# Kernel tuning notes

Measured on AMD Instinct MI355X. Metric: run time of the kernel, lower is better.

The kernel has to match this reference:

```python
import jax, jax.numpy as jnp
import numpy as np

TEMP = 0.1
EPS = 1e-9  # torch CosineSimilarity eps


def setup_inputs() -> dict:
    key = jax.random.key(0)
    k1, k2 = jax.random.split(key)
    h = jax.random.normal(k1, (16384, 2048), dtype=jnp.float32)
    W = jax.random.normal(k2, (512, 2048), dtype=jnp.float32) * (1.0 / np.sqrt(2048))
    return {"h": h, "W": W}


def reference(h, W):
    # process_reps: h already 2D -> identity. Split into anchor / context halves.
    B = h.shape[0] // 2
    wz = h[:B] @ W.T      # [B, low_rank_dim]
    wc = h[B:] @ W.T      # [B, low_rank_dim]

    # CosineSimilarity(dim=-1, eps=1e-9): dot / max(||z||*||c||, eps), pairwise BxB
    nz = jnp.linalg.norm(wz, axis=-1)  # [B]
    nc = jnp.linalg.norm(wc, axis=-1)  # [B]
    sim = (wz @ wc.T) / jnp.maximum(nz[:, None] * nc[None, :], EPS)  # [B, B]
    sim = sim / TEMP

    sim_mean = sim.mean()
    sim_pos = jnp.diagonal(sim).mean()
    logprob = -jax.nn.log_softmax(sim, axis=1)
    loss = jnp.diagonal(logprob).mean()
    # matches loss_dict entries: {'loss', 'loss_pos', 'loss_neg'}
    return jnp.stack([loss, sim_pos, sim_mean])
```

## Files before the change

kernel.cpp:

```cpp
#include <hip/hip_runtime.h>


typedef __attribute__((ext_vector_type(8))) short bf16x8;
typedef __attribute__((ext_vector_type(4))) float floatx4;
typedef unsigned char uchar;

__device__ __forceinline__ unsigned short f2bf(float f) {
    union { float f; unsigned u; } v; v.f = f;
    unsigned r = (v.u + 0x7FFFu + ((v.u >> 16) & 1u)) >> 16;
    return (unsigned short)r;
}

__device__ __forceinline__ void async_copy16(const void* g, void* l) {
    __builtin_amdgcn_global_load_lds(
        (const __attribute__((address_space(1))) void*)g,
        (__attribute__((address_space(3))) void*)l,
        16, 0, 0);
}

__global__ __launch_bounds__(256) void cast_fp8_kernel(
    const float* __restrict__ src, uchar* __restrict__ dst, int n, float scale)
{
    const int i = (blockIdx.x * 256 + threadIdx.x) * 8;
    if (i + 7 < n) {
        float4 a = *reinterpret_cast<const float4*>(src + i);
        float4 b = *reinterpret_cast<const float4*>(src + i + 4);
        const int p01 = __builtin_amdgcn_cvt_pk_fp8_f32(a.x * scale, a.y * scale, 0, 0);
        const int p23 = __builtin_amdgcn_cvt_pk_fp8_f32(a.z * scale, a.w * scale, 0, 0);
        const int p45 = __builtin_amdgcn_cvt_pk_fp8_f32(b.x * scale, b.y * scale, 0, 0);
        const int p67 = __builtin_amdgcn_cvt_pk_fp8_f32(b.z * scale, b.w * scale, 0, 0);
        int2 w;
        w.x = (p01 & 0xffff) | (p23 << 16);
        w.y = (p45 & 0xffff) | (p67 << 16);
        *reinterpret_cast<int2*>(dst + i) = w;
    }
}

__device__ __forceinline__ size_t fl_off(int row_g, int col_g) {
    const int g = row_g >> 4, r15 = row_g & 15;
    const int c = col_g >> 5, q = (col_g >> 3) & 3, b = col_g & 7;
    return ((size_t)g * 16 + c) * 512 + (size_t)(q * 16 + r15) * 8 + b;
}

__global__ __launch_bounds__(256) void g1_main(
    const uchar* __restrict__ h8, const uchar* __restrict__ W8,
    uchar* __restrict__ Z8F, float* __restrict__ norm2)
{
    __shared__ __align__(16) uchar As[128 * 64];
    __shared__ __align__(16) uchar Bs[128 * 64];

    const int o = blockIdx.y * 4 + blockIdx.x;
    const int xcd = o & 7, idx = o >> 3;
    const int bn = idx & 3;
    const int bm = xcd * 16 + (idx >> 2);
    const int t = threadIdx.x;
    const int wave = t >> 6, lane = t & 63;
    const int wm = wave & 1, wn = wave >> 1;
    const int quad = lane >> 4, l15 = lane & 15;

    floatx4 acc[4][4];
    #pragma unroll
    for (int i = 0; i < 4; i++)
        #pragma unroll
        for (int j = 0; j < 4; j++) acc[i][j] = {0.f, 0.f, 0.f, 0.f};

    const int srow0 = wave * 32 + (lane >> 2);
    const int srow1 = srow0 + 16;
    const int p = lane & 3;
    const int sw0 = (p ^ ((srow0 >> 1) & 3)) << 4;
    const int sw1 = (p ^ ((srow1 >> 1) & 3)) << 4;
    const uchar* gA0 = h8 + (size_t)(bm * 128 + srow0) * 2048 + sw0;
    const uchar* gA1 = h8 + (size_t)(bm * 128 + srow1) * 2048 + sw1;
    const uchar* gB0 = W8 + (size_t)(bn * 128 + srow0) * 2048 + sw0;
    const uchar* gB1 = W8 + (size_t)(bn * 128 + srow1) * 2048 + sw1;
    uchar* lA0 = &As[(wave * 32 +  0) * 64];
    uchar* lA1 = &As[(wave * 32 + 16) * 64];
    uchar* lB0 = &Bs[(wave * 32 +  0) * 64];
    uchar* lB1 = &Bs[(wave * 32 + 16) * 64];

    for (int k0 = 0; k0 < 2048; k0 += 64) {
        async_copy16(gA0 + k0, lA0);
        async_copy16(gA1 + k0, lA1);
        async_copy16(gB0 + k0, lB0);
        async_copy16(gB1 + k0, lB1);
        __syncthreads();
        #pragma unroll
        for (int ch = 0; ch < 2; ch++) {
            const int s = ch * 2 + (quad >> 1);
            const int sub = (quad & 1) * 8;
            long a[4], b[4];
            #pragma unroll
            for (int i = 0; i < 4; i++) {
                const int row = wm * 64 + i * 16 + l15;
                a[i] = *reinterpret_cast<const long*>(
                    &As[row * 64 + ((s ^ ((row >> 1) & 3)) << 4) + sub]);
            }
            #pragma unroll
            for (int j = 0; j < 4; j++) {
                const int row = wn * 64 + j * 16 + l15;
                b[j] = *reinterpret_cast<const long*>(
                    &Bs[row * 64 + ((s ^ ((row >> 1) & 3)) << 4) + sub]);
            }
            #pragma unroll
            for (int i = 0; i < 4; i++)
                #pragma unroll
                for (int j = 0; j < 4; j++)
                    acc[i][j] = __builtin_amdgcn_mfma_f32_16x16x32_fp8_fp8(
                        a[i], b[j], acc[i][j], 0, 0, 0);
        }
        __syncthreads();
    }

    #pragma unroll
    for (int i = 0; i < 4; i++) {
        #pragma unroll
        for (int r = 0; r < 4; r++) {
            const int row_g = bm * 128 + wm * 64 + i * 16 + quad * 4 + r;
            const int pk01 = __builtin_amdgcn_cvt_pk_fp8_f32(acc[i][0][r], acc[i][1][r], 0, 0);
            const int pk23 = __builtin_amdgcn_cvt_pk_fp8_f32(acc[i][2][r], acc[i][3][r], 0, 0);
            const uchar q8[4] = { (uchar)(pk01 & 0xff), (uchar)((pk01 >> 8) & 0xff),
                                  (uchar)(pk23 & 0xff), (uchar)((pk23 >> 8) & 0xff) };
            #pragma unroll
            for (int j = 0; j < 4; j++) {
                const int col_g = bn * 128 + wn * 64 + j * 16 + l15;
                Z8F[fl_off(row_g, col_g)] = q8[j];
            }
            const float q0 = __builtin_amdgcn_cvt_f32_fp8(pk01, 0);
            const float q1 = __builtin_amdgcn_cvt_f32_fp8(pk01, 1);
            const float q2 = __builtin_amdgcn_cvt_f32_fp8(pk23, 0);
            const float q3 = __builtin_amdgcn_cvt_f32_fp8(pk23, 1);
            float pw = q0 * q0 + q1 * q1 + q2 * q2 + q3 * q3;
            pw += __shfl_xor(pw, 1, 16);
            pw += __shfl_xor(pw, 2, 16);
            pw += __shfl_xor(pw, 4, 16);
            pw += __shfl_xor(pw, 8, 16);
            if (l15 == 0) atomicAdd(&norm2[row_g], pw);
        }
    }
}

__global__ __launch_bounds__(256) void g1_slow(
    const float* __restrict__ h, const float* __restrict__ W,
    uchar* __restrict__ Z8F, float* __restrict__ norm2)
{
    __shared__ __align__(16) unsigned short As[128][40];
    __shared__ __align__(16) unsigned short Bs[128][40];

    const int bn = blockIdx.x, bm = blockIdx.y;
    const int t = threadIdx.x;
    const int wave = t >> 6, lane = t & 63;
    const int wm = wave & 1, wn = wave >> 1;
    const int quad = lane >> 4, l15 = lane & 15;

    floatx4 acc[4][4];
    #pragma unroll
    for (int i = 0; i < 4; i++)
        #pragma unroll
        for (int j = 0; j < 4; j++) acc[i][j] = {0.f, 0.f, 0.f, 0.f};

    const int lrow = t >> 1, lhalf = t & 1;
    const float* ga = h + (size_t)(bm * 128 + lrow) * 2048 + lhalf * 16;
    const float* gb = W + (size_t)(bn * 128 + lrow) * 2048 + lhalf * 16;

    for (int k0 = 0; k0 < 2048; k0 += 32) {
        #pragma unroll
        for (int c = 0; c < 4; c++) {
            const float4 va = *reinterpret_cast<const float4*>(ga + k0 + c * 4);
            const float4 vb = *reinterpret_cast<const float4*>(gb + k0 + c * 4);
            ushort4 ua = make_ushort4(f2bf(va.x), f2bf(va.y), f2bf(va.z), f2bf(va.w));
            ushort4 ub = make_ushort4(f2bf(vb.x), f2bf(vb.y), f2bf(vb.z), f2bf(vb.w));
            *reinterpret_cast<ushort4*>(&As[lrow][lhalf * 16 + c * 4]) = ua;
            *reinterpret_cast<ushort4*>(&Bs[lrow][lhalf * 16 + c * 4]) = ub;
        }
        __syncthreads();
        bf16x8 af[4], bfr[4];
        #pragma unroll
        for (int i = 0; i < 4; i++)
            af[i] = *reinterpret_cast<const bf16x8*>(&As[wm * 64 + i * 16 + l15][quad * 8]);
        #pragma unroll
        for (int j = 0; j < 4; j++)
            bfr[j] = *reinterpret_cast<const bf16x8*>(&Bs[wn * 64 + j * 16 + l15][quad * 8]);
        #pragma unroll
        for (int i = 0; i < 4; i++)
            #pragma unroll
            for (int j = 0; j < 4; j++)
                acc[i][j] = __builtin_amdgcn_mfma_f32_16x16x32_bf16(af[i], bfr[j], acc[i][j], 0, 0, 0);
        __syncthreads();
    }

    #pragma unroll
    for (int i = 0; i < 4; i++) {
        #pragma unroll
        for (int r = 0; r < 4; r++) {
            const int row_g = bm * 128 + wm * 64 + i * 16 + quad * 4 + r;
            const int pk01 = __builtin_amdgcn_cvt_pk_fp8_f32(acc[i][0][r], acc[i][1][r], 0, 0);
            const int pk23 = __builtin_amdgcn_cvt_pk_fp8_f32(acc[i][2][r], acc[i][3][r], 0, 0);
            const uchar q8[4] = { (uchar)(pk01 & 0xff), (uchar)((pk01 >> 8) & 0xff),
                                  (uchar)(pk23 & 0xff), (uchar)((pk23 >> 8) & 0xff) };
            #pragma unroll
            for (int j = 0; j < 4; j++) {
                const int col_g = bn * 128 + wn * 64 + j * 16 + l15;
                Z8F[fl_off(row_g, col_g)] = q8[j];
            }
            const float q0 = __builtin_amdgcn_cvt_f32_fp8(pk01, 0);
            const float q1 = __builtin_amdgcn_cvt_f32_fp8(pk01, 1);
            const float q2 = __builtin_amdgcn_cvt_f32_fp8(pk23, 0);
            const float q3 = __builtin_amdgcn_cvt_f32_fp8(pk23, 1);
            float pw = q0 * q0 + q1 * q1 + q2 * q2 + q3 * q3;
            pw += __shfl_xor(pw, 1, 16);
            pw += __shfl_xor(pw, 2, 16);
            pw += __shfl_xor(pw, 4, 16);
            pw += __shfl_xor(pw, 8, 16);
            if (l15 == 0) atomicAdd(&norm2[row_g], pw);
        }
    }
}

__global__ __launch_bounds__(256, 4) void g2_main(
    const uchar* __restrict__ Z8F, const float* __restrict__ norm2,
    float* __restrict__ rowse, float* __restrict__ bsum, float* __restrict__ bdiag)
{
    __shared__ float lds_red[2][128][19];
    __shared__ float red[8];

    const int o = blockIdx.y * 64 + blockIdx.x;
    const int xcd = o & 7, idx = o >> 3;
    const int bg = idx >> 7, r = idx & 127;
    const int bm = xcd * 8 + (r >> 4);
    const int bn = bg * 16 + (r & 15);
    const int t = threadIdx.x;
    const int wave = t >> 6, lane = t & 63;
    const int wm = wave & 1, wn = wave >> 1;
    const int quad = lane >> 4, l15 = lane & 15;

    floatx4 acc[4][4];
    #pragma unroll
    for (int i = 0; i < 4; i++)
        #pragma unroll
        for (int j = 0; j < 4; j++) acc[i][j] = {0.f, 0.f, 0.f, 0.f};

    const uchar* baseA = Z8F + ((size_t)(bm * 8 + wm * 4) * 16) * 512 + lane * 8;
    const uchar* baseB = Z8F + ((size_t)(512 + bn * 8 + wn * 4) * 16) * 512 + lane * 8;

    long a[2][4], b[2][4];
    #pragma unroll
    for (int i = 0; i < 4; i++) {
        a[0][i] = *reinterpret_cast<const long*>(baseA + i * 8192);
        b[0][i] = *reinterpret_cast<const long*>(baseB + i * 8192);
    }
    #pragma unroll
    for (int c = 0; c < 16; c++) {
        const int cur = c & 1, nxt = cur ^ 1;
        if (c < 15) {
            #pragma unroll
            for (int i = 0; i < 4; i++) {
                a[nxt][i] = *reinterpret_cast<const long*>(baseA + i * 8192 + (c + 1) * 512);
                b[nxt][i] = *reinterpret_cast<const long*>(baseB + i * 8192 + (c + 1) * 512);
            }
        }
        __builtin_amdgcn_s_setprio(1);
        #pragma unroll
        for (int i = 0; i < 4; i++)
            #pragma unroll
            for (int j = 0; j < 4; j++)
                acc[i][j] = __builtin_amdgcn_mfma_f32_16x16x32_fp8_fp8(
                    a[cur][i], b[cur][j], acc[i][j], 0, 0, 0);
        __builtin_amdgcn_s_setprio(0);
    }

    float rc4[4];
    #pragma unroll
    for (int j = 0; j < 4; j++)
        rc4[j] = rsqrtf(fmaxf(norm2[8192 + bn * 128 + wn * 64 + j * 16 + l15], 1e-30f));

    const bool diagblk = (bm == bn) && (wm == wn);
    float s_tot2 = 0.f, s_diag2 = 0.f;
    #pragma unroll
    for (int i = 0; i < 4; i++) {
        #pragma unroll
        for (int rr = 0; rr < 4; rr++) {
            const int row_t = wm * 64 + i * 16 + quad * 4 + rr;
            const float rzl2 = rsqrtf(fmaxf(norm2[bm * 128 + row_t], 1e-30f)) * 14.4269504089f;
            float rx = 0.f;
            #pragma unroll
            for (int j = 0; j < 4; j++) {
                const float sim2 = acc[i][j][rr] * rzl2 * rc4[j];
                s_tot2 += sim2;
                rx += exp2f(sim2);
            }
            lds_red[wn][row_t][l15] = rx;
            if (diagblk) {
                const float sdv = acc[i][i][rr] * rzl2 * rc4[i];
                s_diag2 += (l15 == quad * 4 + rr) ? sdv : 0.f;
            }
        }
    }
    __syncthreads();

    {
        const int row_t = t >> 1, part = t & 1;
        float v = 0.f;
        #pragma unroll
        for (int c = 0; c < 16; c++) v += lds_red[part][row_t][c];
        v += __shfl_xor(v, 1, 64);
        if (part == 0) atomicAdd(&rowse[bm * 128 + row_t], v);
    }

    #pragma unroll
    for (int off = 32; off; off >>= 1) {
        s_tot2  += __shfl_xor(s_tot2, off, 64);
        s_diag2 += __shfl_xor(s_diag2, off, 64);
    }
    if (lane == 0) { red[wave] = s_tot2; red[4 + wave] = s_diag2; }
    __syncthreads();
    if (t == 0) {
        bsum[bm * 64 + bn]  = (red[0] + red[1] + red[2] + red[3]) * 0.69314718056f;
        bdiag[bm * 64 + bn] = (red[4] + red[5] + red[6] + red[7]) * 0.69314718056f;
    }
}

__global__ __launch_bounds__(256) void finalize_kernel(
    const float* __restrict__ rowse, const float* __restrict__ bsum,
    const float* __restrict__ bdiag, float* __restrict__ out)
{
    float a = 0.f, b = 0.f, c = 0.f;
    for (int i = threadIdx.x; i < 8192; i += 256) a += logf(rowse[i]);
    for (int i = threadIdx.x; i < 4096; i += 256) { b += bsum[i]; c += bdiag[i]; }
    #pragma unroll
    for (int off = 32; off; off >>= 1) {
        a += __shfl_xor(a, off, 64);
        b += __shfl_xor(b, off, 64);
        c += __shfl_xor(c, off, 64);
    }
    __shared__ float ra[4], rb[4], rc[4];
    const int wave = threadIdx.x >> 6, lane = threadIdx.x & 63;
    if (lane == 0) { ra[wave] = a; rb[wave] = b; rc[wave] = c; }
    __syncthreads();
    if (threadIdx.x == 0) {
        const float A = ra[0] + ra[1] + ra[2] + ra[3];
        const float B = rb[0] + rb[1] + rb[2] + rb[3];
        const float C = rc[0] + rc[1] + rc[2] + rc[3];
        const float diag_mean = C / 8192.f;
        out[0] = A / 8192.f - diag_mean;
        out[1] = diag_mean;
        out[2] = B / (8192.f * 8192.f);
    }
}

extern "C" void kernel_launch(void* const* d_in, const int* in_sizes, int n_in,
                              void* d_out, int out_size, void* d_ws, size_t ws_size,
                              hipStream_t stream) {
    const float* h = (const float*)d_in[0];
    const float* W = (const float*)d_in[1];
    float* out = (float*)d_out;

    char* ws = (char*)d_ws;
    float* norm2 = (float*)(ws);
    float* rowse = (float*)(ws + 65536);
    float* bsum  = (float*)(ws + 98304);
    float* bdiag = (float*)(ws + 114688);
    uchar* Z8F   = (uchar*)(ws + 131072);
    uchar* W8    = (uchar*)(ws + 8519680);
    uchar* h8    = (uchar*)(ws + 9568256);
    const size_t NEED_FAST = 43122688ull;

    hipMemsetAsync(ws, 0, 131072, stream);

    if (ws_size >= NEED_FAST) {
        const int nh = 16384 * 2048, nw = 512 * 2048;
        hipLaunchKernelGGL(cast_fp8_kernel, dim3(nh / 2048), dim3(256), 0, stream, h, h8, nh, 1.0f);
        hipLaunchKernelGGL(cast_fp8_kernel, dim3(nw / 2048), dim3(256), 0, stream, W, W8, nw, 32.0f);
        hipLaunchKernelGGL(g1_main, dim3(4, 128), dim3(256), 0, stream, h8, W8, Z8F, norm2);
    } else {
        hipLaunchKernelGGL(g1_slow, dim3(4, 128), dim3(256), 0, stream, h, W, Z8F, norm2);
    }
    hipLaunchKernelGGL(g2_main, dim3(64, 64), dim3(256), 0, stream, Z8F, norm2, rowse, bsum, bdiag);
    hipLaunchKernelGGL(finalize_kernel, dim3(1), dim3(256), 0, stream, rowse, bsum, bdiag, out);
}
```

Measured before the change: 316.5 us.

## Stage B tile in LDS via async copies and repartition waves along M

Each wave previously loaded its own A and B fragments straight from global memory in a 2x2 wave grid. Now the whole 128-row B tile is staged into LDS with async global-to-LDS copies in two halves over K, so all four waves share it. Each wave owns 32 rows of A across all 128 columns, loaded from global with a three-deep register prefetch. This cuts redundant global loads of B, but adds LDS traffic and two barriers in the middle of the K loop where the second half is loaded.

```diff
diff --git a/kernel.cpp b/kernel.cpp
--- a/kernel.cpp
+++ b/kernel.cpp
@@ -220,8 +220,9 @@
     const uchar* __restrict__ Z8F, const float* __restrict__ norm2,
     float* __restrict__ rowse, float* __restrict__ bsum, float* __restrict__ bdiag)
 {
-    __shared__ float lds_red[2][128][19];
+    __shared__ __align__(16) uchar Bs[32768];
     __shared__ float red[8];
+    float (*lds_red)[20] = (float (*)[20])(void*)Bs;
 
     const int o = blockIdx.y * 64 + blockIdx.x;
     const int xcd = o & 7, idx = o >> 3;
@@ -230,80 +231,96 @@
     const int bn = bg * 16 + (r & 15);
     const int t = threadIdx.x;
     const int wave = t >> 6, lane = t & 63;
-    const int wm = wave & 1, wn = wave >> 1;
     const int quad = lane >> 4, l15 = lane & 15;
 
-    floatx4 acc[4][4];
-    #pragma unroll
-    for (int i = 0; i < 4; i++)
-        #pragma unroll
-        for (int j = 0; j < 4; j++) acc[i][j] = {0.f, 0.f, 0.f, 0.f};
-
-    const uchar* baseA = Z8F + ((size_t)(bm * 8 + wm * 4) * 16) * 512 + lane * 8;
-    const uchar* baseB = Z8F + ((size_t)(512 + bn * 8 + wn * 4) * 16) * 512 + lane * 8;
-
-    long a[2][4], b[2][4];
-    #pragma unroll
-    for (int i = 0; i < 4; i++) {
-        a[0][i] = *reinterpret_cast<const long*>(baseA + i * 8192);
-        b[0][i] = *reinterpret_cast<const long*>(baseB + i * 8192);
-    }
+    const uchar* gB = Z8F + (size_t)(512 + bn * 8) * 8192 + t * 16;
+    #pragma unroll
+    for (int s = 0; s < 8; s++)
+        async_copy16(gB + s * 8192, &Bs[s * 4096 + wave * 1024]);
+
+    floatx4 acc[2][8];
+    #pragma unroll
+    for (int i = 0; i < 2; i++)
+        #pragma unroll
+        for (int j = 0; j < 8; j++) acc[i][j] = {0.f, 0.f, 0.f, 0.f};
+
+    const uchar* baseA = Z8F + (size_t)(bm * 8 + wave * 2) * 8192 + lane * 8;
+
+    long ab[3][2];
+    #pragma unroll
+    for (int d = 0; d < 2; d++)
+        #pragma unroll
+        for (int i = 0; i < 2; i++)
+            ab[d][i] = *reinterpret_cast<const long*>(baseA + i * 8192 + d * 512);
+
+    __syncthreads();
+
     #pragma unroll
     for (int c = 0; c < 16; c++) {
-        const int cur = c & 1, nxt = cur ^ 1;
-        if (c < 15) {
-            #pragma unroll
-            for (int i = 0; i < 4; i++) {
-                a[nxt][i] = *reinterpret_cast<const long*>(baseA + i * 8192 + (c + 1) * 512);
-                b[nxt][i] = *reinterpret_cast<const long*>(baseB + i * 8192 + (c + 1) * 512);
-            }
-        }
+        const int cl = c & 7;
+        if (c < 14) {
+            #pragma unroll
+            for (int i = 0; i < 2; i++)
+                ab[(c + 2) % 3][i] = *reinterpret_cast<const long*>(
+                    baseA + i * 8192 + (c + 2) * 512);
+        }
+        long bb[8];
+        #pragma unroll
+        for (int j = 0; j < 8; j++)
+            bb[j] = *reinterpret_cast<const long*>(&Bs[j * 4096 + cl * 512 + lane * 8]);
         __builtin_amdgcn_s_setprio(1);
         #pragma unroll
-        for (int i = 0; i < 4; i++)
-            #pragma unroll
-            for (int j = 0; j < 4; j++)
+        for (int i = 0; i < 2; i++)
+            #pragma unroll
+            for (int j = 0; j < 8; j++)
                 acc[i][j] = __builtin_amdgcn_mfma_f32_16x16x32_fp8_fp8(
-                    a[cur][i], b[cur][j], acc[i][j], 0, 0, 0);
+                    ab[c % 3][i], bb[j], acc[i][j], 0, 0, 0);
         __builtin_amdgcn_s_setprio(0);
-    }
-
-    float rc4[4];
-    #pragma unroll
-    for (int j = 0; j < 4; j++)
-        rc4[j] = rsqrtf(fmaxf(norm2[8192 + bn * 128 + wn * 64 + j * 16 + l15], 1e-30f));
-
-    const bool diagblk = (bm == bn) && (wm == wn);
+        if (c == 7) {
+            __syncthreads();
+            #pragma unroll
+            for (int s = 0; s < 8; s++)
+                async_copy16(gB + s * 8192 + 4096, &Bs[s * 4096 + wave * 1024]);
+            __syncthreads();
+        }
+    }
+
+    __syncthreads();
+
+    float rc8[8];
+    #pragma unroll
+    for (int j = 0; j < 8; j++)
+        rc8[j] = rsqrtf(fmaxf(norm2[8192 + bn * 128 + j * 16 + l15], 1e-30f));
+
+    const bool diagblk = (bm == bn);
     float s_tot2 = 0.f, s_diag2 = 0.f;
     #pragma unroll
-    for (int i = 0; i < 4; i++) {
+    for (int i = 0; i < 2; i++) {
         #pragma unroll
         for (int rr = 0; rr < 4; rr++) {
-            const int row_t = wm * 64 + i * 16 + quad * 4 + rr;
+            const int row_t = wave * 32 + i * 16 + quad * 4 + rr;
             const float rzl2 = rsqrtf(fmaxf(norm2[bm * 128 + row_t], 1e-30f)) * 14.4269504089f;
             float rx = 0.f;
             #pragma unroll
-            for (int j = 0; j < 4; j++) {
-                const float sim2 = acc[i][j][rr] * rzl2 * rc4[j];
+            for (int j = 0; j < 8; j++) {
+                const float sim2 = acc[i][j][rr] * rzl2 * rc8[j];
                 s_tot2 += sim2;
                 rx += exp2f(sim2);
-            }
-            lds_red[wn][row_t][l15] = rx;
-            if (diagblk) {
-                const float sdv = acc[i][i][rr] * rzl2 * rc4[i];
-                s_diag2 += (l15 == quad * 4 + rr) ? sdv : 0.f;
-            }
+                if (diagblk && j == wave * 2 + i && l15 == quad * 4 + rr)
+                    s_diag2 += sim2;
+            }
+            lds_red[row_t][l15] = rx;
         }
     }
     __syncthreads();
 
     {
-        const int row_t = t >> 1, part = t & 1;
+        const int row = t >> 1, half = t & 1;
         float v = 0.f;
         #pragma unroll
-        for (int c = 0; c < 16; c++) v += lds_red[part][row_t][c];
+        for (int cc = 0; cc < 8; cc++) v += lds_red[row][half * 8 + cc];
         v += __shfl_xor(v, 1, 64);
-        if (part == 0) atomicAdd(&rowse[bm * 128 + row_t], v);
+        if (half == 0) atomicAdd(&rowse[bm * 128 + row], v);
     }
 
     #pragma unroll
```

After: 291.7 us. -7.8%, faster.
